# Performance work log

Measured on AMD Instinct MI355X. Metric: run time of the kernel, lower is better.

The kernel has to match this reference:

```python
import jax, jax.numpy as jnp
import numpy as np

N = 50000   # nodes
E = 800000  # edges (before self-loops)
D = 128     # d_model == in_dim
H = 8       # heads
C = D // H  # per-head channels = 16
NEG_SLOPE = 0.2  # PyG GATConv default


def gat_conv(x, row, col, W, a_src, a_dst, bias):
    # x: [N, Din]; row/col: [E'] src/dst with self-loops; W: [Din, H*C]
    h = (x @ W).reshape(N, H, C)                       # [N, H, C]
    alpha_src = (h * a_src).sum(-1)                    # [N, H]
    alpha_dst = (h * a_dst).sum(-1)                    # [N, H]
    e = jax.nn.leaky_relu(alpha_src[row] + alpha_dst[col], NEG_SLOPE)  # [E', H]
    # segment softmax over incoming edges of each dst node (col)
    e_max = jax.ops.segment_max(e, col, num_segments=N)               # [N, H]
    e_exp = jnp.exp(e - e_max[col])                                   # [E', H]
    denom = jax.ops.segment_sum(e_exp, col, num_segments=N)           # [N, H]
    alpha = e_exp / (denom[col] + 1e-16)                              # [E', H]
    msg = h[row] * alpha[:, :, None]                                  # [E', H, C]
    out = jax.ops.segment_sum(msg, col, num_segments=N)               # [N, H, C]
    return out.reshape(N, H * C) + bias


def setup_inputs() -> dict:
    key = jax.random.key(0)
    ks = jax.random.split(key, 14)
    s = 0.05
    return {
        "x": jax.random.normal(ks[0], (N, D), dtype=jnp.float32),
        "edge_index": jax.random.randint(ks[1], (2, E), 0, N, dtype=jnp.int64),
        "pos": jax.random.normal(ks[2], (N, 3), dtype=jnp.float32),
        "W1": jax.random.normal(ks[3], (D, H * C), dtype=jnp.float32) * s,
        "a_src1": jax.random.normal(ks[4], (H, C), dtype=jnp.float32) * s,
        "a_dst1": jax.random.normal(ks[5], (H, C), dtype=jnp.float32) * s,
        "b1": jnp.zeros((H * C,), dtype=jnp.float32),
        "W2": jax.random.normal(ks[6], (D, H * C), dtype=jnp.float32) * s,
        "a_src2": jax.random.normal(ks[7], (H, C), dtype=jnp.float32) * s,
        "a_dst2": jax.random.normal(ks[8], (H, C), dtype=jnp.float32) * s,
        "b2": jnp.zeros((H * C,), dtype=jnp.float32),
        "Wd": jax.random.normal(ks[9], (1, D), dtype=jnp.float32) * s,
        "bd": jnp.zeros((D,), dtype=jnp.float32),
    }


def reference(x, edge_index, pos, W1, a_src1, a_dst1, b1, W2, a_src2, a_dst2, b2, Wd, bd):
    row, col = edge_index[0], edge_index[1]
    # dist embedding (computed in source forward, not used in the returned sum)
    dist = jnp.linalg.norm(pos[row] - pos[col], axis=1, keepdims=True)  # [E, 1]
    dist_emb = jax.nn.relu(dist @ Wd + bd)  # noqa: F841 (unused, as in source)
    # GATConv adds self-loops internally (PyG default add_self_loops=True)
    loop = jnp.arange(N, dtype=row.dtype)
    row_sl = jnp.concatenate([row, loop])
    col_sl = jnp.concatenate([col, loop])
    h1 = jax.nn.relu(gat_conv(x, row_sl, col_sl, W1, a_src1, a_dst1, b1))
    h2 = jax.nn.relu(gat_conv(h1, row_sl, col_sl, W2, a_src2, a_dst2, b2))
    return x + h1 + h2
```

## Files before the change

kernel.cpp:

```cpp
#include <hip/hip_runtime.h>
#include <hip/hip_bf16.h>
#include <math.h>


constexpr int D = 128;
constexpr int CAP = 64;
constexpr int WPACK = 18432;

using bf16x8 = __attribute__((ext_vector_type(8))) short;
using f32x4 = __attribute__((ext_vector_type(4))) float;

static __device__ __forceinline__ float lrelu(float v) {
  return v > 0.f ? v : 0.2f * v;
}

static __device__ __forceinline__ ushort bfbits(float f) {
  __hip_bfloat16 b = __float2bfloat16(f);
  return *reinterpret_cast<ushort*>(&b);
}

static __device__ __forceinline__ float bf2f(ushort u) {
  union { unsigned int u; float f; } c;
  c.u = (unsigned int)u << 16;
  return c.f;
}

__global__ void pack_all_kernel(const float* __restrict__ W1, const float* __restrict__ as1,
                                const float* __restrict__ ad1, ushort* __restrict__ wp1,
                                const float* __restrict__ W2, const float* __restrict__ as2,
                                const float* __restrict__ ad2, ushort* __restrict__ wp2,
                                int* __restrict__ cnt, int N) {
  int t = blockIdx.x * blockDim.x + threadIdx.x;
  if (t < N) cnt[t] = 0;
  const float *W, *as_, *ad_;
  ushort* wp;
  int idx;
  if (t < WPACK) {
    W = W1; as_ = as1; ad_ = ad1; wp = wp1; idx = t;
  } else if (t < 2 * WPACK) {
    W = W2; as_ = as2; ad_ = ad2; wp = wp2; idx = t - WPACK;
  } else {
    return;
  }
  if (idx < 16384) {
    int e = idx & 7, c = (idx >> 3) & 15, ct = (idx >> 7) & 7, g = (idx >> 10) & 3,
        ks = idx >> 12;
    int k = ks * 32 + g * 8 + e, n = ct * 16 + c;
    wp[idx] = bfbits(W[k * 128 + n]);
  } else {
    int j = idx - 16384;
    int e = j & 7, c = (j >> 3) & 15, g = (j >> 7) & 3, ks = j >> 9;
    int k = ks * 32 + g * 8 + e;
    int h = c & 7;
    const float* a = (c >> 3) ? ad_ : as_;
    float s = 0.f;
    #pragma unroll
    for (int cc = 0; cc < 16; ++cc) s += W[k * 128 + h * 16 + cc] * a[h * 16 + cc];
    wp[idx] = bfbits(s);
  }
}

template <bool BF_IN, bool SCATTER>
__global__ __launch_bounds__(256) void gemm_mfma_kernel(
    const void* __restrict__ Xv, const ushort* __restrict__ Wp,
    ushort* __restrict__ Hf, ushort* __restrict__ asrc, float* __restrict__ adst,
    int N, const int* __restrict__ row, const int* __restrict__ col,
    int* __restrict__ cnt, ushort* __restrict__ csr_pad, int E, int gemmBlocks) {
  if (SCATTER && (int)blockIdx.x >= gemmBlocks) {
    int e = ((int)blockIdx.x - gemmBlocks) * 256 + (int)threadIdx.x;
    if (e < E) {
      int c = col[e];
      int p = atomicAdd(&cnt[c], 1);
      if (p < CAP) csr_pad[(size_t)c * CAP + p] = (ushort)row[e];
    }
    return;
  }

  __shared__ ushort Wl[WPACK];
  int tid = threadIdx.x;
  for (int i = tid; i < WPACK / 8; i += 256)
    *(uint4*)&Wl[i * 8] = *(const uint4*)&Wp[i * 8];
  __syncthreads();

  int lane = tid & 63, w = tid >> 6;
  int g = lane >> 4, c = lane & 15;
  int rt0 = blockIdx.x * 128 + w * 32;

  f32x4 acc[2][9];
  #pragma unroll
  for (int rt = 0; rt < 2; ++rt)
    #pragma unroll
    for (int ct = 0; ct < 9; ++ct) acc[rt][ct] = (f32x4)0.f;

  #pragma unroll
  for (int ks = 0; ks < 4; ++ks) {
    bf16x8 a[2];
    #pragma unroll
    for (int rt = 0; rt < 2; ++rt) {
      int r = rt0 + rt * 16 + c;
      if (r < N) {
        if (BF_IN) {
          a[rt] = *(const bf16x8*)&((const ushort*)Xv)[(size_t)r * D + ks * 32 + g * 8];
        } else {
          const float* xp = &((const float*)Xv)[(size_t)r * D + ks * 32 + g * 8];
          float4 x0 = *(const float4*)xp;
          float4 x1 = *(const float4*)(xp + 4);
          bf16x8 t;
          t[0] = (short)bfbits(x0.x); t[1] = (short)bfbits(x0.y);
          t[2] = (short)bfbits(x0.z); t[3] = (short)bfbits(x0.w);
          t[4] = (short)bfbits(x1.x); t[5] = (short)bfbits(x1.y);
          t[6] = (short)bfbits(x1.z); t[7] = (short)bfbits(x1.w);
          a[rt] = t;
        }
      } else {
        a[rt] = (bf16x8)(short)0;
      }
    }
    #pragma unroll
    for (int ct = 0; ct < 9; ++ct) {
      const ushort* bp = (ct < 8)
          ? &Wl[(size_t)(((ks * 4 + g) * 8 + ct) * 16 + c) * 8]
          : &Wl[16384 + (size_t)((ks * 4 + g) * 16 + c) * 8];
      bf16x8 b = *(const bf16x8*)bp;
      acc[0][ct] = __builtin_amdgcn_mfma_f32_16x16x32_bf16(a[0], b, acc[0][ct], 0, 0, 0);
      acc[1][ct] = __builtin_amdgcn_mfma_f32_16x16x32_bf16(a[1], b, acc[1][ct], 0, 0, 0);
    }
  }

  #pragma unroll
  for (int rt = 0; rt < 2; ++rt) {
    #pragma unroll
    for (int j = 0; j < 4; ++j) {
      int r = rt0 + rt * 16 + g * 4 + j;
      if (r >= N) continue;
      #pragma unroll
      for (int ct = 0; ct < 8; ++ct)
        Hf[(size_t)r * D + ct * 16 + c] = bfbits(acc[rt][ct][j]);
      float lv = acc[rt][8][j];
      if (c < 8) asrc[r * 8 + c] = bfbits(lv);
      else adst[r * 8 + (c - 8)] = lv;
    }
  }
}

template <int LAYER>
__global__ __launch_bounds__(256) void aggregate_kernel(
    const ushort* __restrict__ Hf, const ushort* __restrict__ asrc,
    const float* __restrict__ adst, const int* __restrict__ cnt,
    const ushort* __restrict__ csr_pad, const float* __restrict__ bias,
    const float* __restrict__ xin, const ushort* __restrict__ h1in,
    void* __restrict__ outp, int N) {
  int wid = (blockIdx.x * blockDim.x + threadIdx.x) >> 6;
  if (wid >= N) return;
  int lane = threadIdx.x & 63;
  int h = lane >> 3;
  int d0 = lane * 2;
  int dst = wid;
  float adst_h = adst[dst * 8 + h];
  float ws = __expf(lrelu(bf2f(asrc[dst * 8 + h]) + adst_h));
  ushort2 fs = *(const ushort2*)&Hf[(size_t)dst * D + d0];
  float accx = ws * bf2f(fs.x), accy = ws * bf2f(fs.y), wsum = ws;
  int cn = min(cnt[dst], CAP);
  const ushort* cp = csr_pad + (size_t)dst * CAP;
  int i = 0;
  for (; i + 4 <= cn; i += 4) {
    ushort4 s4 = *(const ushort4*)(cp + i);
    float l0 = bf2f(asrc[(int)s4.x * 8 + h]);
    float l1 = bf2f(asrc[(int)s4.y * 8 + h]);
    float l2 = bf2f(asrc[(int)s4.z * 8 + h]);
    float l3 = bf2f(asrc[(int)s4.w * 8 + h]);
    ushort2 f0 = *(const ushort2*)&Hf[(size_t)s4.x * D + d0];
    ushort2 f1 = *(const ushort2*)&Hf[(size_t)s4.y * D + d0];
    ushort2 f2 = *(const ushort2*)&Hf[(size_t)s4.z * D + d0];
    ushort2 f3 = *(const ushort2*)&Hf[(size_t)s4.w * D + d0];
    float w0 = __expf(lrelu(l0 + adst_h));
    float w1 = __expf(lrelu(l1 + adst_h));
    float w2 = __expf(lrelu(l2 + adst_h));
    float w3 = __expf(lrelu(l3 + adst_h));
    accx += w0 * bf2f(f0.x) + w1 * bf2f(f1.x) + w2 * bf2f(f2.x) + w3 * bf2f(f3.x);
    accy += w0 * bf2f(f0.y) + w1 * bf2f(f1.y) + w2 * bf2f(f2.y) + w3 * bf2f(f3.y);
    wsum += w0 + w1 + w2 + w3;
  }
  for (; i < cn; ++i) {
    int src = cp[i];
    float we = __expf(lrelu(bf2f(asrc[src * 8 + h]) + adst_h));
    ushort2 fv = *(const ushort2*)&Hf[(size_t)src * D + d0];
    accx += we * bf2f(fv.x);
    accy += we * bf2f(fv.y);
    wsum += we;
  }
  float inv = 1.f / (wsum + 1e-16f);
  float2 bv = *(const float2*)&bias[d0];
  float r0 = fmaxf(accx * inv + bv.x, 0.f);
  float r1 = fmaxf(accy * inv + bv.y, 0.f);
  if (LAYER == 1) {
    ushort2 u;
    u.x = bfbits(r0); u.y = bfbits(r1);
    *(ushort2*)&((ushort*)outp)[(size_t)dst * D + d0] = u;
  } else {
    float2 xv = *(const float2*)&xin[(size_t)dst * D + d0];
    ushort2 hv = *(const ushort2*)&h1in[(size_t)dst * D + d0];
    *(float2*)&((float*)outp)[(size_t)dst * D + d0] =
        make_float2(xv.x + bf2f(hv.x) + r0, xv.y + bf2f(hv.y) + r1);
  }
}

extern "C" void kernel_launch(void* const* d_in, const int* in_sizes, int n_in,
                              void* d_out, int out_size, void* d_ws, size_t ws_size,
                              hipStream_t stream) {
  const float* x = (const float*)d_in[0];
  const int* ei = (const int*)d_in[1];
  const float* W1 = (const float*)d_in[3];
  const float* as1 = (const float*)d_in[4];
  const float* ad1 = (const float*)d_in[5];
  const float* b1 = (const float*)d_in[6];
  const float* W2 = (const float*)d_in[7];
  const float* as2 = (const float*)d_in[8];
  const float* ad2 = (const float*)d_in[9];
  const float* b2 = (const float*)d_in[10];
  float* out = (float*)d_out;

  const int N = in_sizes[0] / D;
  const int E = in_sizes[1] / 2;
  const int* row = ei;
  const int* col = ei + E;

  char* base = (char*)d_ws;
  size_t o = 0;
  auto alloc = [&](size_t bytes) {
    void* p = base + o;
    o = (o + bytes + 255) & ~(size_t)255;
    return p;
  };
  int* cnt = (int*)alloc((size_t)N * 4);
  ushort* csr_pad = (ushort*)alloc((size_t)N * CAP * 2);
  ushort* hf = (ushort*)alloc((size_t)N * D * 2);
  ushort* h1 = (ushort*)alloc((size_t)N * D * 2);
  ushort* asrcb = (ushort*)alloc((size_t)N * 8 * 2);
  float* adstb = (float*)alloc((size_t)N * 8 * 4);
  ushort* wp1 = (ushort*)alloc((size_t)WPACK * 2);
  ushort* wp2 = (ushort*)alloc((size_t)WPACK * 2);

  int gemm_blocks = (N + 127) / 128;
  int scat_blocks = (E + 255) / 256;
  int agg_blocks = (N + 3) / 4;
  int prep_threads = 2 * WPACK > N ? 2 * WPACK : N;

  pack_all_kernel<<<(prep_threads + 255) / 256, 256, 0, stream>>>(
      W1, as1, ad1, wp1, W2, as2, ad2, wp2, cnt, N);
  gemm_mfma_kernel<false, true><<<gemm_blocks + scat_blocks, 256, 0, stream>>>(
      x, wp1, hf, asrcb, adstb, N, row, col, cnt, csr_pad, E, gemm_blocks);
  aggregate_kernel<1><<<agg_blocks, 256, 0, stream>>>(hf, asrcb, adstb, cnt, csr_pad,
                                                      b1, nullptr, nullptr, h1, N);
  gemm_mfma_kernel<true, false><<<gemm_blocks, 256, 0, stream>>>(
      h1, wp2, hf, asrcb, adstb, N, nullptr, nullptr, nullptr, nullptr, 0, gemm_blocks);
  aggregate_kernel<2><<<agg_blocks, 256, 0, stream>>>(hf, asrcb, adstb, cnt, csr_pad,
                                                      b2, x, h1, out, N);
}
```

Measured before the change: 245.2 us.

## Bucket edges by destination block and fuse layer-1 aggregation with layer-2 GEMM

CSR construction becomes two passes. Edges are first binned into 1024-node buckets, using shared-memory histograms and one global atomic per block per bucket. A second pass then builds each bucket's padded adjacency lists with shared-memory atomics, in place of one global atomic per edge. Layer-1 aggregation is fused with the layer-2 projection GEMM: each block aggregates 32 nodes into LDS and runs MFMA on them directly, so the separate GEMM launch and the h1 reread disappear. The cost is an extra bucket pass with a fixed bucket capacity that can silently drop edges, and the fused kernel has lower GEMM efficiency because it reads weights from global memory and leaves three of four waves idle on the attention column tile.

After: 260.3 us. +6.1%, slower.

```diff
diff --git a/kernel.cpp b/kernel.cpp
--- a/kernel.cpp
+++ b/kernel.cpp
@@ -6,6 +6,9 @@
 constexpr int D = 128;
 constexpr int CAP = 64;
 constexpr int WPACK = 18432;
+constexpr int NBMAX = 64;
+constexpr int BCAP = 24576;
+constexpr int EPB = 4096;
 
 using bf16x8 = __attribute__((ext_vector_type(8))) short;
 using f32x4 = __attribute__((ext_vector_type(4))) float;
@@ -29,9 +32,9 @@
                                 const float* __restrict__ ad1, ushort* __restrict__ wp1,
                                 const float* __restrict__ W2, const float* __restrict__ as2,
                                 const float* __restrict__ ad2, ushort* __restrict__ wp2,
-                                int* __restrict__ cnt, int N) {
+                                int* __restrict__ bucket_cnt) {
   int t = blockIdx.x * blockDim.x + threadIdx.x;
-  if (t < N) cnt[t] = 0;
+  if (t < NBMAX) bucket_cnt[t] = 0;
   const float *W, *as_, *ad_;
   ushort* wp;
   int idx;
@@ -60,31 +63,73 @@
   }
 }
 
-template <bool BF_IN, bool SCATTER>
-__global__ __launch_bounds__(256) void gemm_mfma_kernel(
-    const void* __restrict__ Xv, const ushort* __restrict__ Wp,
+__global__ __launch_bounds__(256) void bucket_kernel(
+    const int* __restrict__ row, const int* __restrict__ col,
+    int* __restrict__ bucket_cnt, unsigned int* __restrict__ bkt, int E, int NB) {
+  __shared__ int hist[NBMAX];
+  __shared__ int base_s[NBMAX];
+  int tid = threadIdx.x;
+  if (tid < NBMAX) hist[tid] = 0;
+  __syncthreads();
+  int e0 = blockIdx.x * EPB;
+  unsigned int uv[16];
+  int bb[16], rr[16];
+  #pragma unroll
+  for (int j = 0; j < 16; ++j) {
+    int e = e0 + j * 256 + tid;
+    bb[j] = -1; uv[j] = 0; rr[j] = 0;
+    if (e < E) {
+      int c = col[e], r = row[e];
+      bb[j] = c >> 10;
+      uv[j] = ((unsigned int)(c & 1023) << 16) | (unsigned int)r;
+      rr[j] = atomicAdd(&hist[bb[j]], 1);
+    }
+  }
+  __syncthreads();
+  if (tid < NB) base_s[tid] = atomicAdd(&bucket_cnt[tid], hist[tid]);
+  __syncthreads();
+  #pragma unroll
+  for (int j = 0; j < 16; ++j) {
+    if (bb[j] >= 0) {
+      int pos = base_s[bb[j]] + rr[j];
+      if (pos < BCAP) bkt[(size_t)bb[j] * BCAP + pos] = uv[j];
+    }
+  }
+}
+
+__global__ __launch_bounds__(256) void csr_gemm_kernel(
+    const float* __restrict__ X, const ushort* __restrict__ Wp,
     ushort* __restrict__ Hf, ushort* __restrict__ asrc, float* __restrict__ adst,
-    int N, const int* __restrict__ row, const int* __restrict__ col,
-    int* __restrict__ cnt, ushort* __restrict__ csr_pad, int E, int gemmBlocks) {
-  if (SCATTER && (int)blockIdx.x >= gemmBlocks) {
-    int e = ((int)blockIdx.x - gemmBlocks) * 256 + (int)threadIdx.x;
-    if (e < E) {
-      int c = col[e];
-      int p = atomicAdd(&cnt[c], 1);
-      if (p < CAP) csr_pad[(size_t)c * CAP + p] = (ushort)row[e];
-    }
-    return;
-  }
-
+    int N, const unsigned int* __restrict__ bkt, const int* __restrict__ bucket_cnt,
+    int* __restrict__ cnt, ushort* __restrict__ csr_pad, int NB) {
   __shared__ ushort Wl[WPACK];
   int tid = threadIdx.x;
+  if ((int)blockIdx.x < NB) {
+    int b = blockIdx.x;
+    int* lcnt = (int*)Wl;
+    for (int i = tid; i < 1024; i += 256) lcnt[i] = 0;
+    __syncthreads();
+    int ce = min(bucket_cnt[b], BCAP);
+    const unsigned int* bp = bkt + (size_t)b * BCAP;
+    for (int i = tid; i < ce; i += 256) {
+      unsigned int u = bp[i];
+      int dl = u >> 16;
+      int p = atomicAdd(&lcnt[dl], 1);
+      if (p < CAP) csr_pad[((size_t)((b << 10) + dl)) * CAP + p] = (ushort)(u & 0xffffu);
+    }
+    __syncthreads();
+    int nd = min(1024, N - (b << 10));
+    for (int i = tid; i < nd; i += 256) cnt[(b << 10) + i] = lcnt[i];
+    return;
+  }
+
   for (int i = tid; i < WPACK / 8; i += 256)
     *(uint4*)&Wl[i * 8] = *(const uint4*)&Wp[i * 8];
   __syncthreads();
 
   int lane = tid & 63, w = tid >> 6;
   int g = lane >> 4, c = lane & 15;
-  int rt0 = blockIdx.x * 128 + w * 32;
+  int rt0 = ((int)blockIdx.x - NB) * 128 + w * 32;
 
   f32x4 acc[2][9];
   #pragma unroll
@@ -99,19 +144,15 @@
     for (int rt = 0; rt < 2; ++rt) {
       int r = rt0 + rt * 16 + c;
       if (r < N) {
-        if (BF_IN) {
-          a[rt] = *(const bf16x8*)&((const ushort*)Xv)[(size_t)r * D + ks * 32 + g * 8];
-        } else {
-          const float* xp = &((const float*)Xv)[(size_t)r * D + ks * 32 + g * 8];
-          float4 x0 = *(const float4*)xp;
-          float4 x1 = *(const float4*)(xp + 4);
-          bf16x8 t;
-          t[0] = (short)bfbits(x0.x); t[1] = (short)bfbits(x0.y);
-          t[2] = (short)bfbits(x0.z); t[3] = (short)bfbits(x0.w);
-          t[4] = (short)bfbits(x1.x); t[5] = (short)bfbits(x1.y);
-          t[6] = (short)bfbits(x1.z); t[7] = (short)bfbits(x1.w);
-          a[rt] = t;
-        }
+        const float* xp = &X[(size_t)r * D + ks * 32 + g * 8];
+        float4 x0 = *(const float4*)xp;
+        float4 x1 = *(const float4*)(xp + 4);
+        bf16x8 t;
+        t[0] = (short)bfbits(x0.x); t[1] = (short)bfbits(x0.y);
+        t[2] = (short)bfbits(x0.z); t[3] = (short)bfbits(x0.w);
+        t[4] = (short)bfbits(x1.x); t[5] = (short)bfbits(x1.y);
+        t[6] = (short)bfbits(x1.z); t[7] = (short)bfbits(x1.w);
+        a[rt] = t;
       } else {
         a[rt] = (bf16x8)(short)0;
       }
@@ -143,23 +184,13 @@
   }
 }
 
-template <int LAYER>
-__global__ __launch_bounds__(256) void aggregate_kernel(
-    const ushort* __restrict__ Hf, const ushort* __restrict__ asrc,
-    const float* __restrict__ adst, const int* __restrict__ cnt,
-    const ushort* __restrict__ csr_pad, const float* __restrict__ bias,
-    const float* __restrict__ xin, const ushort* __restrict__ h1in,
-    void* __restrict__ outp, int N) {
-  int wid = (blockIdx.x * blockDim.x + threadIdx.x) >> 6;
-  if (wid >= N) return;
-  int lane = threadIdx.x & 63;
-  int h = lane >> 3;
-  int d0 = lane * 2;
-  int dst = wid;
-  float adst_h = adst[dst * 8 + h];
+static __device__ __forceinline__ void gather_node(
+    const ushort* __restrict__ Hf, const ushort* __restrict__ asrc, float adst_h,
+    const int* __restrict__ cnt, const ushort* __restrict__ csr_pad,
+    int dst, int h, int d0, float& accx, float& accy, float& wsum) {
   float ws = __expf(lrelu(bf2f(asrc[dst * 8 + h]) + adst_h));
   ushort2 fs = *(const ushort2*)&Hf[(size_t)dst * D + d0];
-  float accx = ws * bf2f(fs.x), accy = ws * bf2f(fs.y), wsum = ws;
+  accx = ws * bf2f(fs.x); accy = ws * bf2f(fs.y); wsum = ws;
   int cn = min(cnt[dst], CAP);
   const ushort* cp = csr_pad + (size_t)dst * CAP;
   int i = 0;
@@ -189,20 +220,116 @@
     accy += we * bf2f(fv.y);
     wsum += we;
   }
-  float inv = 1.f / (wsum + 1e-16f);
-  float2 bv = *(const float2*)&bias[d0];
-  float r0 = fmaxf(accx * inv + bv.x, 0.f);
-  float r1 = fmaxf(accy * inv + bv.y, 0.f);
-  if (LAYER == 1) {
+}
+
+__global__ __launch_bounds__(256) void agg_gemm_kernel(
+    const ushort* __restrict__ Hf1, const ushort* __restrict__ asrc1,
+    const float* __restrict__ adst1, const int* __restrict__ cnt,
+    const ushort* __restrict__ csr_pad, const float* __restrict__ bias1,
+    const ushort* __restrict__ wp2, ushort* __restrict__ h1out,
+    ushort* __restrict__ Hf2, ushort* __restrict__ asrc2, float* __restrict__ adst2,
+    int N) {
+  __shared__ ushort Ht[32][144];
+  int tid = threadIdx.x, lane = tid & 63, w = tid >> 6;
+  int h = lane >> 3, d0 = lane * 2;
+  int dst0 = blockIdx.x * 32;
+
+  for (int i = 0; i < 8; ++i) {
+    int trow = w * 8 + i;
+    int dst = dst0 + trow;
+    float r0 = 0.f, r1 = 0.f;
+    if (dst < N) {
+      float adh = adst1[dst * 8 + h];
+      float ax, ay, wsm;
+      gather_node(Hf1, asrc1, adh, cnt, csr_pad, dst, h, d0, ax, ay, wsm);
+      float inv = 1.f / (wsm + 1e-16f);
+      float2 bv = *(const float2*)&bias1[d0];
+      r0 = fmaxf(ax * inv + bv.x, 0.f);
+      r1 = fmaxf(ay * inv + bv.y, 0.f);
+    }
     ushort2 u;
     u.x = bfbits(r0); u.y = bfbits(r1);
-    *(ushort2*)&((ushort*)outp)[(size_t)dst * D + d0] = u;
-  } else {
-    float2 xv = *(const float2*)&xin[(size_t)dst * D + d0];
-    ushort2 hv = *(const ushort2*)&h1in[(size_t)dst * D + d0];
-    *(float2*)&((float*)outp)[(size_t)dst * D + d0] =
-        make_float2(xv.x + bf2f(hv.x) + r0, xv.y + bf2f(hv.y) + r1);
-  }
+    *(ushort2*)&Ht[trow][d0] = u;
+    if (dst < N) *(ushort2*)&h1out[(size_t)dst * D + d0] = u;
+  }
+  __syncthreads();
+
+  int g = lane >> 4, c = lane & 15;
+  bf16x8 afr[2][4];
+  #pragma unroll
+  for (int rt = 0; rt < 2; ++rt)
+    #pragma unroll
+    for (int ks = 0; ks < 4; ++ks)
+      afr[rt][ks] = *(const bf16x8*)&Ht[rt * 16 + c][ks * 32 + g * 8];
+
+  f32x4 acc[2][3];
+  #pragma unroll
+  for (int rt = 0; rt < 2; ++rt)
+    #pragma unroll
+    for (int ci = 0; ci < 3; ++ci) acc[rt][ci] = (f32x4)0.f;
+
+  #pragma unroll
+  for (int ci = 0; ci < 3; ++ci) {
+    bool act = (ci < 2) || (w == 0);
+    if (!act) continue;
+    int ct = (ci == 0) ? w : (ci == 1) ? (4 + w) : 8;
+    #pragma unroll
+    for (int ks = 0; ks < 4; ++ks) {
+      const ushort* bp = (ct < 8)
+          ? &wp2[(size_t)(((ks * 4 + g) * 8 + ct) * 16 + c) * 8]
+          : &wp2[16384 + (size_t)((ks * 4 + g) * 16 + c) * 8];
+      bf16x8 b = *(const bf16x8*)bp;
+      acc[0][ci] = __builtin_amdgcn_mfma_f32_16x16x32_bf16(afr[0][ks], b, acc[0][ci], 0, 0, 0);
+      acc[1][ci] = __builtin_amdgcn_mfma_f32_16x16x32_bf16(afr[1][ks], b, acc[1][ci], 0, 0, 0);
+    }
+  }
+
+  #pragma unroll
+  for (int ci = 0; ci < 3; ++ci) {
+    bool act = (ci < 2) || (w == 0);
+    if (!act) continue;
+    int ct = (ci == 0) ? w : (ci == 1) ? (4 + w) : 8;
+    #pragma unroll
+    for (int rt = 0; rt < 2; ++rt) {
+      #pragma unroll
+      for (int j = 0; j < 4; ++j) {
+        int r = rt * 16 + g * 4 + j;
+        int dst = dst0 + r;
+        if (dst >= N) continue;
+        float lv = acc[rt][ci][j];
+        if (ct < 8) {
+          Hf2[(size_t)dst * D + ct * 16 + c] = bfbits(lv);
+        } else {
+          if (c < 8) asrc2[dst * 8 + c] = bfbits(lv);
+          else adst2[dst * 8 + (c - 8)] = lv;
+        }
+      }
+    }
+  }
+}
+
+__global__ __launch_bounds__(256) void aggregate2_kernel(
+    const ushort* __restrict__ Hf, const ushort* __restrict__ asrc,
+    const float* __restrict__ adst, const int* __restrict__ cnt,
+    const ushort* __restrict__ csr_pad, const float* __restrict__ bias,
+    const float* __restrict__ xin, const ushort* __restrict__ h1in,
+    float* __restrict__ outp, int N) {
+  int wid = (blockIdx.x * blockDim.x + threadIdx.x) >> 6;
+  if (wid >= N) return;
+  int lane = threadIdx.x & 63;
+  int h = lane >> 3, d0 = lane * 2;
+  int dst = wid;
+  float adh = adst[dst * 8 + h];
+  float ax, ay, wsm;
+  gather_node(Hf, asrc, adh, cnt, csr_pad, dst, h, d0, ax, ay, wsm);
+  float inv = 1.f / (wsm + 1e-16f);
+  float2 bv = *(const float2*)&bias[d0];
+  float r0 = fmaxf(ax * inv + bv.x, 0.f);
+  float r1 = fmaxf(ay * inv + bv.y, 0.f);
+  float2 xv = *(const float2*)&xin[(size_t)dst * D + d0];
+  ushort2 hv = *(const ushort2*)&h1in[(size_t)dst * D + d0];
+  *(float2*)&outp[(size_t)dst * D + d0] =
+      make_float2(xv.x + bf2f(hv.x) + r0, xv.y + bf2f(hv.y) + r1);
 }
 
 extern "C" void kernel_launch(void* const* d_in, const int* in_sizes, int n_in,
@@ -224,6 +351,7 @@
   const int E = in_sizes[1] / 2;
   const int* row = ei;
   const int* col = ei + E;
+  const int NB = (N + 1023) >> 10;
 
   char* base = (char*)d_ws;
   size_t o = 0;
@@ -232,28 +360,29 @@
     o = (o + bytes + 255) & ~(size_t)255;
     return p;
   };
+  int* bucket_cnt = (int*)alloc((size_t)NBMAX * 4);
+  unsigned int* bkt = (unsigned int*)alloc((size_t)NBMAX * BCAP * 4);
   int* cnt = (int*)alloc((size_t)N * 4);
   ushort* csr_pad = (ushort*)alloc((size_t)N * CAP * 2);
-  ushort* hf = (ushort*)alloc((size_t)N * D * 2);
+  ushort* hf1 = (ushort*)alloc((size_t)N * D * 2);
+  ushort* hf2 = (ushort*)alloc((size_t)N * D * 2);
   ushort* h1 = (ushort*)alloc((size_t)N * D * 2);
-  ushort* asrcb = (ushort*)alloc((size_t)N * 8 * 2);
-  float* adstb = (float*)alloc((size_t)N * 8 * 4);
+  ushort* asrc1 = (ushort*)alloc((size_t)N * 8 * 2);
+  ushort* asrc2 = (ushort*)alloc((size_t)N * 8 * 2);
+  float* adst1 = (float*)alloc((size_t)N * 8 * 4);
+  float* adst2 = (float*)alloc((size_t)N * 8 * 4);
   ushort* wp1 = (ushort*)alloc((size_t)WPACK * 2);
   ushort* wp2 = (ushort*)alloc((size_t)WPACK * 2);
 
   int gemm_blocks = (N + 127) / 128;
-  int scat_blocks = (E + 255) / 256;
-  int agg_blocks = (N + 3) / 4;
-  int prep_threads = 2 * WPACK > N ? 2 * WPACK : N;
-
-  pack_all_kernel<<<(prep_threads + 255) / 256, 256, 0, stream>>>(
-      W1, as1, ad1, wp1, W2, as2, ad2, wp2, cnt, N);
-  gemm_mfma_kernel<false, true><<<gemm_blocks + scat_blocks, 256, 0, stream>>>(
-      x, wp1, hf, asrcb, adstb, N, row, col, cnt, csr_pad, E, gemm_blocks);
-  aggregate_kernel<1><<<agg_blocks, 256, 0, stream>>>(hf, asrcb, adstb, cnt, csr_pad,
-                                                      b1, nullptr, nullptr, h1, N);
-  gemm_mfma_kernel<true, false><<<gemm_blocks, 256, 0, stream>>>(
-      h1, wp2, hf, asrcb, adstb, N, nullptr, nullptr, nullptr, nullptr, 0, gemm_blocks);
-  aggregate_kernel<2><<<agg_blocks, 256, 0, stream>>>(hf, asrcb, adstb, cnt, csr_pad,
-                                                      b2, x, h1, out, N);
-}
+
+  pack_all_kernel<<<(2 * WPACK + 255) / 256, 256, 0, stream>>>(
+      W1, as1, ad1, wp1, W2, as2, ad2, wp2, bucket_cnt);
+  bucket_kernel<<<(E + EPB - 1) / EPB, 256, 0, stream>>>(row, col, bucket_cnt, bkt, E, NB);
+  csr_gemm_kernel<<<NB + gemm_blocks, 256, 0, stream>>>(
+      x, wp1, hf1, asrc1, adst1, N, bkt, bucket_cnt, cnt, csr_pad, NB);
+  agg_gemm_kernel<<<(N + 31) / 32, 256, 0, stream>>>(
+      hf1, asrc1, adst1, cnt, csr_pad, b1, wp2, h1, hf2, asrc2, adst2, N);
+  aggregate2_kernel<<<(N + 3) / 4, 256, 0, stream>>>(
+      hf2, asrc2, adst2, cnt, csr_pad, b2, x, h1, out, N);
+}
```
